# Kernel tuning notes

Hardware: AMD Instinct MI355X
Metric: run time of the kernel (lower is better)

Reference implementation:

```python
import jax, jax.numpy as jnp
import numpy as np

K = 20000   # know_num
I = 50000   # item_num
D = 128     # emb_dim
N = K + I   # nodes in exer+know graphs (exercises first)
E1 = 320000 # edges in directed knowledge graph
E2 = 640000 # edges in each exer<->know graph


def setup_inputs() -> dict:
    key = jax.random.key(0)
    ks = jax.random.split(key, 20)
    s = 1.0 / np.sqrt(D)
    s2 = 1.0 / np.sqrt(2 * D)
    return {
        'kn_emb': jax.random.normal(ks[0], (K, D), jnp.float32),
        'exer_emb': jax.random.normal(ks[1], (I, D), jnp.float32),
        # GAT params: W is fc.weight.T ([in,out]); a is attn_fc.weight flattened ([2D])
        'W_dir': jax.random.normal(ks[2], (D, D), jnp.float32) * s,
        'a_dir': jax.random.normal(ks[3], (2 * D,), jnp.float32) * s2,
        'W_ke': jax.random.normal(ks[4], (D, D), jnp.float32) * s,
        'a_ke': jax.random.normal(ks[5], (2 * D,), jnp.float32) * s2,
        'W_ek': jax.random.normal(ks[6], (D, D), jnp.float32) * s,
        'a_ek': jax.random.normal(ks[7], (2 * D,), jnp.float32) * s2,
        # relation attention MLP: Linear(D,D)+bias, Tanh, Linear(D,1,no bias)
        'rel_W1': jax.random.normal(ks[8], (D, D), jnp.float32) * s,
        'rel_b1': jax.random.normal(ks[9], (D,), jnp.float32) * s,
        'rel_w2': jax.random.normal(ks[10], (D,), jnp.float32) * s,
        # edge lists (src, dst)
        'directed_src': jax.random.randint(ks[11], (E1,), 0, K),
        'directed_dst': jax.random.randint(ks[12], (E1,), 0, K),
        'ke_src': jax.random.randint(ks[13], (E2,), 0, N),
        'ke_dst': jax.random.randint(ks[14], (E2,), 0, N),
        'ek_src': jax.random.randint(ks[15], (E2,), 0, N),
        'ek_dst': jax.random.randint(ks[16], (E2,), 0, N),
    }


def _gat(h, W, a, src, dst, n):
    # GraphLayer: z = fc(h); e = leaky_relu(attn_fc([z_src; z_dst]));
    # alpha = softmax_e over dst; h_out = sum alpha * z_src
    z = h @ W                                   # [n_in, D]
    # split attn vector: cat([z_src,z_dst]) @ a == z_src@a[:D] + z_dst@a[D:]
    s_src = z @ a[:D]                           # [n_in]
    s_dst = z @ a[D:]                           # [n_in]
    e = jax.nn.leaky_relu(s_src[src] + s_dst[dst], 0.01)  # [E]
    m = jax.ops.segment_max(e, dst, num_segments=n)
    ex = jnp.exp(e - m[dst])
    den = jax.ops.segment_sum(ex, dst, num_segments=n)
    alpha = ex / den[dst]                       # segment softmax over in-edges
    return jax.ops.segment_sum(alpha[:, None] * z[src], dst, num_segments=n)


def reference(kn_emb, exer_emb, W_dir, a_dir, W_ke, a_ke, W_ek, a_ek,
              rel_W1, rel_b1, rel_w2,
              directed_src, directed_dst, ke_src, ke_dst, ek_src, ek_dst):
    A = _gat(kn_emb, W_dir, a_dir, directed_src, directed_dst, K)      # [K,D]
    ek = jnp.concatenate([exer_emb, kn_emb], axis=0)                   # [N,D]
    B = _gat(ek, W_ke, a_ke, ke_src, ke_dst, N)[I:]                    # [K,D]
    Cfull = _gat(ek, W_ek, a_ek, ek_src, ek_dst, N)                    # [N,D]
    s1 = jnp.tanh(A @ rel_W1 + rel_b1) @ rel_w2                        # [K]
    s2 = jnp.tanh(B @ rel_W1 + rel_b1) @ rel_w2                        # [K]
    score = jax.nn.softmax(jnp.stack([s1, s2], axis=1), axis=1)        # [K,2]
    kn_out = score[:, 0:1] * A + score[:, 1:2] * B                     # [K,D]
    exer_out = Cfull[:I]                                               # [I,D]
    return (kn_out, exer_out)
```

## Files before the change

kernel.cpp:

```cpp
#include <hip/hip_runtime.h>
#include <math.h>

#define KN   20000
#define IN_  50000
#define DD   128
#define NN   70000
#define E1N  320000
#define E2N  640000

#define GB0  313
#define GB1  1094
#define GB2  1094
#define GTILES 2501

#define GROUPS 313
#define MGRID  (GROUPS*13)
#define CNT_CHUNKS 1563

typedef _Float16 f16x8 __attribute__((ext_vector_type(8)));
typedef float floatx4 __attribute__((ext_vector_type(4)));

__device__ __forceinline__ unsigned f2bf(float x) {
  unsigned u = __float_as_uint(x);
  return (u + 0x7FFFu + ((u >> 16) & 1u)) >> 16;
}
__device__ __forceinline__ unsigned packbf(float a, float b) {
  return f2bf(a) | (f2bf(b) << 16);
}
__device__ __forceinline__ float bf_lo(unsigned u) { return __uint_as_float(u << 16); }
__device__ __forceinline__ float bf_hi(unsigned u) { return __uint_as_float(u & 0xFFFF0000u); }

__global__ __launch_bounds__(256) void prep(
    const float* __restrict__ W0, const float* __restrict__ W1,
    const float* __restrict__ W2, const float* __restrict__ W3,
    short* __restrict__ wfr)
{
  int b = blockIdx.x;
  int wsel = b >> 3;
  const float* W = (wsel == 0) ? W0 : (wsel == 1) ? W1 : (wsel == 2) ? W2 : W3;
  int fi = (b & 7) * 256 + threadIdx.x;
  int l = fi & 63, chunk = (fi >> 6) & 3, t = fi >> 8;
  int col = t * 16 + (l & 15);
  int kbase = chunk * 32 + (l >> 4) * 8;
  f16x8 hv;
#pragma unroll
  for (int j = 0; j < 8; ++j) hv[j] = (_Float16)W[(kbase + j) * 128 + col];
  ((f16x8*)(wfr + wsel * 16384))[fi] = hv;
}

__global__ __launch_bounds__(256, 4) void gemm3_count(
    const float* __restrict__ kn, const float* __restrict__ ex,
    const short* __restrict__ wfr,
    const float* __restrict__ a_dir, const float* __restrict__ a_ke, const float* __restrict__ a_ek,
    unsigned* __restrict__ zb_dir, unsigned* __restrict__ zb_ke, unsigned* __restrict__ zb_ek,
    float* __restrict__ sds, float* __restrict__ sdd,
    float* __restrict__ sks, float* __restrict__ skd,
    float* __restrict__ ses, float* __restrict__ sed,
    const int* __restrict__ ddst, const int* __restrict__ kedst, const int* __restrict__ ekdst,
    int* __restrict__ cnt_dir, int* __restrict__ cnt_ke, int* __restrict__ cnt_ek,
    unsigned short* __restrict__ rank_dir, unsigned short* __restrict__ rank_ke,
    unsigned short* __restrict__ rank_ek)
{
  __shared__ short sW[16384];
  const int g = blockIdx.x / 13;
  const int r = blockIdx.x % 13;
  const int tid = threadIdx.x;

  if (r >= 8) {
    int cidx = g * 5 + (r - 8);
    if (cidx >= CNT_CHUNKS) return;
    int t = cidx * 256 + tid;
    if (t < 80000) {
      int e0 = t * 4;
      int4 d4 = *(const int4*)(ddst + e0);
      ushort4 rk;
      rk.x = (unsigned short)atomicAdd(&cnt_dir[d4.x], 1);
      rk.y = (unsigned short)atomicAdd(&cnt_dir[d4.y], 1);
      rk.z = (unsigned short)atomicAdd(&cnt_dir[d4.z], 1);
      rk.w = (unsigned short)atomicAdd(&cnt_dir[d4.w], 1);
      *(ushort4*)(rank_dir + e0) = rk;
    } else if (t < 240000) {
      int e0 = (t - 80000) * 4;
      int4 d4 = *(const int4*)(kedst + e0);
      ushort4 rk = make_ushort4(0, 0, 0, 0);
      if (d4.x >= IN_) rk.x = (unsigned short)atomicAdd(&cnt_ke[d4.x - IN_], 1);
      if (d4.y >= IN_) rk.y = (unsigned short)atomicAdd(&cnt_ke[d4.y - IN_], 1);
      if (d4.z >= IN_) rk.z = (unsigned short)atomicAdd(&cnt_ke[d4.z - IN_], 1);
      if (d4.w >= IN_) rk.w = (unsigned short)atomicAdd(&cnt_ke[d4.w - IN_], 1);
      *(ushort4*)(rank_ke + e0) = rk;
    } else if (t < 400000) {
      int e0 = (t - 240000) * 4;
      int4 d4 = *(const int4*)(ekdst + e0);
      ushort4 rk = make_ushort4(0, 0, 0, 0);
      if (d4.x < IN_) rk.x = (unsigned short)atomicAdd(&cnt_ek[d4.x], 1);
      if (d4.y < IN_) rk.y = (unsigned short)atomicAdd(&cnt_ek[d4.y], 1);
      if (d4.z < IN_) rk.z = (unsigned short)atomicAdd(&cnt_ek[d4.z], 1);
      if (d4.w < IN_) rk.w = (unsigned short)atomicAdd(&cnt_ek[d4.w], 1);
      *(ushort4*)(rank_ek + e0) = rk;
    }
    return;
  }

  const int bid = g * 8 + r;
  if (bid >= GTILES) return;

  const float *h1, *h2, *avec;
  unsigned* zb;
  float *ssrc, *sdst;
  const short* wf;
  int split, rows, tile;
  if (bid < GB0) {
    tile = bid; rows = KN; split = KN; h1 = kn; h2 = kn;
    wf = wfr; avec = a_dir; zb = zb_dir; ssrc = sds; sdst = sdd;
  } else if (bid < GB0 + GB1) {
    tile = bid - GB0; rows = NN; split = IN_; h1 = ex; h2 = kn;
    wf = wfr + 16384; avec = a_ke; zb = zb_ke; ssrc = sks; sdst = skd;
  } else {
    tile = bid - GB0 - GB1; rows = NN; split = IN_; h1 = ex; h2 = kn;
    wf = wfr + 32768; avec = a_ek; zb = zb_ek; ssrc = ses; sdst = sed;
  }

  {
    const int4* gs = (const int4*)wf;
    int4* ls = (int4*)sW;
#pragma unroll
    for (int it = 0; it < 8; ++it) ls[it * 256 + tid] = gs[it * 256 + tid];
  }
  __syncthreads();

  const int lane = tid & 63;
  const int wv = tid >> 6;
  const int q = lane >> 4;
  const int m = lane & 15;
  const int rr = tile * 64 + wv * 16 + m;
  const int rc = (rr < rows) ? rr : (rows - 1);
  const float* hp = (rc < split) ? (h1 + (size_t)rc * 128)
                                 : (h2 + (size_t)(rc - split) * 128);

  floatx4 acc[8];
#pragma unroll
  for (int t = 0; t < 8; ++t) { acc[t][0]=0.f; acc[t][1]=0.f; acc[t][2]=0.f; acc[t][3]=0.f; }

#pragma unroll
  for (int chunk = 0; chunk < 4; ++chunk) {
    float4 v0 = *(const float4*)(hp + chunk * 32 + q * 8);
    float4 v1 = *(const float4*)(hp + chunk * 32 + q * 8 + 4);
    float vs[8] = {v0.x, v0.y, v0.z, v0.w, v1.x, v1.y, v1.z, v1.w};
    f16x8 ahi, alo;
#pragma unroll
    for (int j = 0; j < 8; ++j) {
      _Float16 h = (_Float16)vs[j];
      ahi[j] = h;
      alo[j] = (_Float16)(vs[j] - (float)h);
    }
#pragma unroll
    for (int t = 0; t < 8; ++t) {
      f16x8 bh = ((const f16x8*)sW)[(t * 4 + chunk) * 64 + lane];
      acc[t] = __builtin_amdgcn_mfma_f32_16x16x32_f16(bh, ahi, acc[t], 0, 0, 0);
      acc[t] = __builtin_amdgcn_mfma_f32_16x16x32_f16(bh, alo, acc[t], 0, 0, 0);
    }
  }

  if (rr < rows) {
    unsigned* zrow = zb + (size_t)rr * 64;
#pragma unroll
    for (int t = 0; t < 8; ++t) {
      uint2 pk;
      pk.x = packbf(acc[t][0], acc[t][1]);
      pk.y = packbf(acc[t][2], acc[t][3]);
      *(uint2*)(zrow + t * 8 + q * 2) = pk;
    }
  }
  float d1 = 0.f, d2 = 0.f;
#pragma unroll
  for (int t = 0; t < 8; ++t) {
    float4 wa = *(const float4*)(avec + t * 16 + q * 4);
    float4 wb = *(const float4*)(avec + 128 + t * 16 + q * 4);
    d1 += acc[t][0] * wa.x + acc[t][1] * wa.y + acc[t][2] * wa.z + acc[t][3] * wa.w;
    d2 += acc[t][0] * wb.x + acc[t][1] * wb.y + acc[t][2] * wb.z + acc[t][3] * wb.w;
  }
  d1 += __shfl_xor(d1, 16, 64); d1 += __shfl_xor(d1, 32, 64);
  d2 += __shfl_xor(d2, 16, 64); d2 += __shfl_xor(d2, 32, 64);
  if (q == 0 && rr < rows) { ssrc[rr] = d1; sdst[rr] = d2; }
}

__global__ __launch_bounds__(256) void alloc_off(
    const int* __restrict__ cnt_dir, int2* __restrict__ sc_dir,
    const int* __restrict__ cnt_ke,  int2* __restrict__ sc_ke,
    const int* __restrict__ cnt_ek,  int2* __restrict__ sc_ek,
    int* __restrict__ totals)
{
  int b = blockIdx.x;
  const int* cnt; int2* sc; int* tot; int n, i0;
  if (b < 79)       { cnt = cnt_dir; sc = sc_dir; tot = totals + 0; n = KN;  i0 = b * 256; }
  else if (b < 158) { cnt = cnt_ke;  sc = sc_ke;  tot = totals + 1; n = KN;  i0 = (b - 79) * 256; }
  else              { cnt = cnt_ek;  sc = sc_ek;  tot = totals + 2; n = IN_; i0 = (b - 158) * 256; }
  int i = i0 + threadIdx.x;
  int lane = threadIdx.x & 63;
  int v = (i < n) ? cnt[i] : 0;
  int x = v;
#pragma unroll
  for (int o = 1; o < 64; o <<= 1) {
    int t = __shfl_up(x, o, 64);
    if (lane >= o) x += t;
  }
  int base = 0;
  if (lane == 63) base = atomicAdd(tot, x);
  base = __shfl(base, 63, 64);
  if (i < n) sc[i] = make_int2(base + x - v, v);
}

__global__ __launch_bounds__(256) void fill_edges(
    const int* __restrict__ dsrc, const int* __restrict__ ddst,
    const int* __restrict__ kesrc, const int* __restrict__ kedst,
    const int* __restrict__ eksrc, const int* __restrict__ ekdst,
    const unsigned short* __restrict__ rank_dir, const unsigned short* __restrict__ rank_ke,
    const unsigned short* __restrict__ rank_ek,
    const float* __restrict__ sds, const float* __restrict__ sdd,
    const float* __restrict__ sks, const float* __restrict__ skd,
    const float* __restrict__ ses, const float* __restrict__ sed,
    const int2* __restrict__ sc_dir, int2* __restrict__ ep_dir,
    const int2* __restrict__ sc_ke,  int2* __restrict__ ep_ke,
    const int2* __restrict__ sc_ek,  int2* __restrict__ ep_ek)
{
  int t = blockIdx.x * 256 + threadIdx.x;
  if (t < 80000) {
    int e0 = t * 4;
    int4 s4 = *(const int4*)(dsrc + e0);
    int4 d4 = *(const int4*)(ddst + e0);
    ushort4 rk = *(const ushort4*)(rank_dir + e0);
    ep_dir[sc_dir[d4.x].x + rk.x] = make_int2(s4.x, __float_as_int(sds[s4.x] + sdd[d4.x]));
    ep_dir[sc_dir[d4.y].x + rk.y] = make_int2(s4.y, __float_as_int(sds[s4.y] + sdd[d4.y]));
    ep_dir[sc_dir[d4.z].x + rk.z] = make_int2(s4.z, __float_as_int(sds[s4.z] + sdd[d4.z]));
    ep_dir[sc_dir[d4.w].x + rk.w] = make_int2(s4.w, __float_as_int(sds[s4.w] + sdd[d4.w]));
  } else if (t < 240000) {
    int e0 = (t - 80000) * 4;
    int4 s4 = *(const int4*)(kesrc + e0);
    int4 d4 = *(const int4*)(kedst + e0);
    ushort4 rk = *(const ushort4*)(rank_ke + e0);
    if (d4.x >= IN_) ep_ke[sc_ke[d4.x - IN_].x + rk.x] = make_int2(s4.x, __float_as_int(sks[s4.x] + skd[d4.x]));
    if (d4.y >= IN_) ep_ke[sc_ke[d4.y - IN_].x + rk.y] = make_int2(s4.y, __float_as_int(sks[s4.y] + skd[d4.y]));
    if (d4.z >= IN_) ep_ke[sc_ke[d4.z - IN_].x + rk.z] = make_int2(s4.z, __float_as_int(sks[s4.z] + skd[d4.z]));
    if (d4.w >= IN_) ep_ke[sc_ke[d4.w - IN_].x + rk.w] = make_int2(s4.w, __float_as_int(sks[s4.w] + skd[d4.w]));
  } else if (t < 400000) {
    int e0 = (t - 240000) * 4;
    int4 s4 = *(const int4*)(eksrc + e0);
    int4 d4 = *(const int4*)(ekdst + e0);
    ushort4 rk = *(const ushort4*)(rank_ek + e0);
    if (d4.x < IN_) ep_ek[sc_ek[d4.x].x + rk.x] = make_int2(s4.x, __float_as_int(ses[s4.x] + sed[d4.x]));
    if (d4.y < IN_) ep_ek[sc_ek[d4.y].x + rk.y] = make_int2(s4.y, __float_as_int(ses[s4.y] + sed[d4.y]));
    if (d4.z < IN_) ep_ek[sc_ek[d4.z].x + rk.z] = make_int2(s4.z, __float_as_int(ses[s4.z] + sed[d4.z]));
    if (d4.w < IN_) ep_ek[sc_ek[d4.w].x + rk.w] = make_int2(s4.w, __float_as_int(ses[s4.w] + sed[d4.w]));
  }
}

__global__ __launch_bounds__(256) void gat_gather(
    const int2* __restrict__ sc_dir, const int2* __restrict__ ep_dir,
    const unsigned* __restrict__ zb_dir, float* __restrict__ A,
    const int2* __restrict__ sc_ke, const int2* __restrict__ ep_ke,
    const unsigned* __restrict__ zb_ke, float* __restrict__ Bm,
    const int2* __restrict__ sc_ek, const int2* __restrict__ ep_ek,
    const unsigned* __restrict__ zb_ek, float* __restrict__ Cout)
{
  int gw = (blockIdx.x * 256 + threadIdx.x) >> 6;
  int lane = threadIdx.x & 63;
  int h = lane >> 5;
  int ln31 = lane & 31;
  int gh = (lane >> 4) & 1;
  int gl = lane & 15;

  const int2 *scp, *ep;
  const unsigned* zb;
  float* out;
  int s0;
  if (gw < 10000)      { s0 = 2 * gw;             scp = sc_dir; ep = ep_dir; zb = zb_dir; out = A; }
  else if (gw < 20000) { s0 = 2 * (gw - 10000);   scp = sc_ke;  ep = ep_ke;  zb = zb_ke;  out = Bm; }
  else                 { s0 = 2 * (gw - 20000);   scp = sc_ek;  ep = ep_ek;  zb = zb_ek;  out = Cout; }

  int4 scc = *(const int4*)((const int*)scp + 2 * s0);
  int b   = h ? scc.z : scc.x;
  int cnt = h ? scc.w : scc.y;
  int lim = (cnt < 32) ? cnt : 32;

  int   src_l = 0;
  float w_l   = 0.f;
  if (ln31 < lim) {
    int2 pe = ep[b + ln31];
    src_l = pe.x;
    float x = __int_as_float(pe.y);
    x = (x > 0.f) ? x : 0.01f * x;
    w_l = __expf(x);
  }

  float den = w_l;
  den += __shfl_xor(den, 1, 64);
  den += __shfl_xor(den, 2, 64);
  den += __shfl_xor(den, 4, 64);
  den += __shfl_xor(den, 8, 64);
  den += __shfl_xor(den, 16, 64);

  float av[8];
#pragma unroll
  for (int k = 0; k < 8; ++k) av[k] = 0.f;

  for (int j0 = 0; j0 < lim; j0 += 8) {
    int base = h * 32 + j0 + gh * 4;
    int   s1 = __shfl(src_l, base + 0, 64); float w1 = __shfl(w_l, base + 0, 64);
    int   s2 = __shfl(src_l, base + 1, 64); float w2 = __shfl(w_l, base + 1, 64);
    int   s3 = __shfl(src_l, base + 2, 64); float w3 = __shfl(w_l, base + 2, 64);
    int   s4 = __shfl(src_l, base + 3, 64); float w4 = __shfl(w_l, base + 3, 64);
    uint4 za = *(const uint4*)(zb + (size_t)s1 * 64 + gl * 4);
    uint4 zc = *(const uint4*)(zb + (size_t)s2 * 64 + gl * 4);
    uint4 ze = *(const uint4*)(zb + (size_t)s3 * 64 + gl * 4);
    uint4 zg = *(const uint4*)(zb + (size_t)s4 * 64 + gl * 4);
    av[0] += w1 * bf_lo(za.x); av[1] += w1 * bf_hi(za.x);
    av[2] += w1 * bf_lo(za.y); av[3] += w1 * bf_hi(za.y);
    av[4] += w1 * bf_lo(za.z); av[5] += w1 * bf_hi(za.z);
    av[6] += w1 * bf_lo(za.w); av[7] += w1 * bf_hi(za.w);
    av[0] += w2 * bf_lo(zc.x); av[1] += w2 * bf_hi(zc.x);
    av[2] += w2 * bf_lo(zc.y); av[3] += w2 * bf_hi(zc.y);
    av[4] += w2 * bf_lo(zc.z); av[5] += w2 * bf_hi(zc.z);
    av[6] += w2 * bf_lo(zc.w); av[7] += w2 * bf_hi(zc.w);
    av[0] += w3 * bf_lo(ze.x); av[1] += w3 * bf_hi(ze.x);
    av[2] += w3 * bf_lo(ze.y); av[3] += w3 * bf_hi(ze.y);
    av[4] += w3 * bf_lo(ze.z); av[5] += w3 * bf_hi(ze.z);
    av[6] += w3 * bf_lo(ze.w); av[7] += w3 * bf_hi(ze.w);
    av[0] += w4 * bf_lo(zg.x); av[1] += w4 * bf_hi(zg.x);
    av[2] += w4 * bf_lo(zg.y); av[3] += w4 * bf_hi(zg.y);
    av[4] += w4 * bf_lo(zg.z); av[5] += w4 * bf_hi(zg.z);
    av[6] += w4 * bf_lo(zg.w); av[7] += w4 * bf_hi(zg.w);
  }

  if (cnt > 32) {
    float dtail = 0.f;
    int e = b + cnt;
    for (int i = b + 32 + gh; i < e; i += 2) {
      int2 p1 = ep[i];
      float x1 = __int_as_float(p1.y);
      x1 = (x1 > 0.f) ? x1 : 0.01f * x1;
      float w1 = __expf(x1);
      uint4 za = *(const uint4*)(zb + (size_t)p1.x * 64 + gl * 4);
      dtail += w1;
      av[0] += w1 * bf_lo(za.x); av[1] += w1 * bf_hi(za.x);
      av[2] += w1 * bf_lo(za.y); av[3] += w1 * bf_hi(za.y);
      av[4] += w1 * bf_lo(za.z); av[5] += w1 * bf_hi(za.z);
      av[6] += w1 * bf_lo(za.w); av[7] += w1 * bf_hi(za.w);
    }
    den += dtail + __shfl_xor(dtail, 16, 64);
  }

#pragma unroll
  for (int k = 0; k < 8; ++k) av[k] += __shfl_xor(av[k], 16, 64);

  if (cnt > 0) {
    float inv = 1.f / den;
#pragma unroll
    for (int k = 0; k < 8; ++k) av[k] *= inv;
  }

  if (gh == 0) {
    int seg = s0 + h;
    float* op = out + (size_t)seg * 128 + gl * 8;
    *(float4*)op       = make_float4(av[0], av[1], av[2], av[3]);
    *(float4*)(op + 4) = make_float4(av[4], av[5], av[6], av[7]);
  }
}

__global__ __launch_bounds__(256, 2) void relgemm_combine(
    const float* __restrict__ Am, const float* __restrict__ Bm,
    const short* __restrict__ wfr_rel,
    const float* __restrict__ rb1, const float* __restrict__ rw2,
    float* __restrict__ out)
{
  __shared__ short sW[16384];
  const int tid = threadIdx.x;
  {
    const int4* gs = (const int4*)wfr_rel;
    int4* ls = (int4*)sW;
#pragma unroll
    for (int it = 0; it < 8; ++it) ls[it * 256 + tid] = gs[it * 256 + tid];
  }
  __syncthreads();

  const int lane = tid & 63;
  const int wv = tid >> 6;
  const int q = lane >> 4;
  const int m = lane & 15;
  const int r = blockIdx.x * 64 + wv * 16 + m;
  const int rc = (r < KN) ? r : (KN - 1);
  const float* hA = Am + (size_t)rc * 128;
  const float* hB = Bm + (size_t)rc * 128;

  floatx4 accA[8], accB[8];
#pragma unroll
  for (int t = 0; t < 8; ++t) {
    accA[t][0]=0.f; accA[t][1]=0.f; accA[t][2]=0.f; accA[t][3]=0.f;
    accB[t][0]=0.f; accB[t][1]=0.f; accB[t][2]=0.f; accB[t][3]=0.f;
  }

#pragma unroll
  for (int chunk = 0; chunk < 4; ++chunk) {
    float4 a0 = *(const float4*)(hA + chunk * 32 + q * 8);
    float4 a1 = *(const float4*)(hA + chunk * 32 + q * 8 + 4);
    float4 b0 = *(const float4*)(hB + chunk * 32 + q * 8);
    float4 b1 = *(const float4*)(hB + chunk * 32 + q * 8 + 4);
    float as[8] = {a0.x, a0.y, a0.z, a0.w, a1.x, a1.y, a1.z, a1.w};
    float bs[8] = {b0.x, b0.y, b0.z, b0.w, b1.x, b1.y, b1.z, b1.w};
    f16x8 ahiA, aloA, ahiB, aloB;
#pragma unroll
    for (int j = 0; j < 8; ++j) {
      _Float16 ha = (_Float16)as[j];
      ahiA[j] = ha; aloA[j] = (_Float16)(as[j] - (float)ha);
      _Float16 hb = (_Float16)bs[j];
      ahiB[j] = hb; aloB[j] = (_Float16)(bs[j] - (float)hb);
    }
#pragma unroll
    for (int t = 0; t < 8; ++t) {
      f16x8 bh = ((const f16x8*)sW)[(t * 4 + chunk) * 64 + lane];
      accA[t] = __builtin_amdgcn_mfma_f32_16x16x32_f16(bh, ahiA, accA[t], 0, 0, 0);
      accA[t] = __builtin_amdgcn_mfma_f32_16x16x32_f16(bh, aloA, accA[t], 0, 0, 0);
      accB[t] = __builtin_amdgcn_mfma_f32_16x16x32_f16(bh, ahiB, accB[t], 0, 0, 0);
      accB[t] = __builtin_amdgcn_mfma_f32_16x16x32_f16(bh, aloB, accB[t], 0, 0, 0);
    }
  }

  float p1 = 0.f, p2 = 0.f;
#pragma unroll
  for (int t = 0; t < 8; ++t) {
    float4 bb = *(const float4*)(rb1 + t * 16 + q * 4);
    float4 ww = *(const float4*)(rw2 + t * 16 + q * 4);
    p1 += tanhf(accA[t][0] + bb.x) * ww.x + tanhf(accA[t][1] + bb.y) * ww.y +
          tanhf(accA[t][2] + bb.z) * ww.z + tanhf(accA[t][3] + bb.w) * ww.w;
    p2 += tanhf(accB[t][0] + bb.x) * ww.x + tanhf(accB[t][1] + bb.y) * ww.y +
          tanhf(accB[t][2] + bb.z) * ww.z + tanhf(accB[t][3] + bb.w) * ww.w;
  }
  p1 += __shfl_xor(p1, 16, 64); p1 += __shfl_xor(p1, 32, 64);
  p2 += __shfl_xor(p2, 16, 64); p2 += __shfl_xor(p2, 32, 64);

  float mx = fmaxf(p1, p2);
  float e1 = __expf(p1 - mx), e2 = __expf(p2 - mx);
  float al = e1 / (e1 + e2), be = e2 / (e1 + e2);

  if (r < KN) {
#pragma unroll
    for (int t = 0; t < 8; ++t) {
      int col = t * 16 + q * 4;
      float4 avv = *(const float4*)(Am + (size_t)r * 128 + col);
      float4 bvv = *(const float4*)(Bm + (size_t)r * 128 + col);
      *(float4*)(out + (size_t)r * 128 + col) =
          make_float4(al * avv.x + be * bvv.x, al * avv.y + be * bvv.y,
                      al * avv.z + be * bvv.z, al * avv.w + be * bvv.w);
    }
  }
}

extern "C" void kernel_launch(void* const* d_in, const int* in_sizes, int n_in,
                              void* d_out, int out_size, void* d_ws, size_t ws_size,
                              hipStream_t stream) {
  const float* kn    = (const float*)d_in[0];
  const float* ex    = (const float*)d_in[1];
  const float* W_dir = (const float*)d_in[2];
  const float* a_dir = (const float*)d_in[3];
  const float* W_ke  = (const float*)d_in[4];
  const float* a_ke  = (const float*)d_in[5];
  const float* W_ek  = (const float*)d_in[6];
  const float* a_ek  = (const float*)d_in[7];
  const float* rW1   = (const float*)d_in[8];
  const float* rb1   = (const float*)d_in[9];
  const float* rw2   = (const float*)d_in[10];
  const int* dsrc    = (const int*)d_in[11];
  const int* ddst    = (const int*)d_in[12];
  const int* kesrc   = (const int*)d_in[13];
  const int* kedst   = (const int*)d_in[14];
  const int* eksrc   = (const int*)d_in[15];
  const int* ekdst   = (const int*)d_in[16];
  float* out = (float*)d_out;

  char* p = (char*)d_ws;
  auto alloc = [&](size_t bytes) {
    char* r = p;
    p += (bytes + 255) & ~(size_t)255;
    return r;
  };
  unsigned* zb_dir = (unsigned*)alloc((size_t)KN * 64 * 4);
  unsigned* zb_ke  = (unsigned*)alloc((size_t)NN * 64 * 4);
  unsigned* zb_ek  = (unsigned*)alloc((size_t)NN * 64 * 4);
  float* Am    = (float*)alloc((size_t)KN * 128 * 4);
  float* Bmat  = (float*)alloc((size_t)KN * 128 * 4);
  short* wfr   = (short*)alloc((size_t)4 * 16384 * 2);
  float* sds = (float*)alloc(KN * 4);
  float* sdd = (float*)alloc(KN * 4);
  float* sks = (float*)alloc(NN * 4);
  float* skd = (float*)alloc(NN * 4);
  float* ses = (float*)alloc(NN * 4);
  float* sed = (float*)alloc(NN * 4);
  int* cntblk  = (int*)alloc((size_t)(2 * KN + IN_ + 64) * 4);
  int* cnt_dir = cntblk;
  int* cnt_ke  = cntblk + KN;
  int* cnt_ek  = cntblk + 2 * KN;
  int* totals  = cntblk + 2 * KN + IN_;
  int2* sc_dir = (int2*)alloc((size_t)KN * 8);
  int2* sc_ke  = (int2*)alloc((size_t)KN * 8);
  int2* sc_ek  = (int2*)alloc((size_t)IN_ * 8);
  unsigned short* rank_dir = (unsigned short*)alloc((size_t)E1N * 2);
  unsigned short* rank_ke  = (unsigned short*)alloc((size_t)E2N * 2);
  unsigned short* rank_ek  = (unsigned short*)alloc((size_t)E2N * 2);
  int2* ep_dir = (int2*)alloc((size_t)E1N * 8);
  int2* ep_ke  = (int2*)alloc((size_t)E2N * 8);
  int2* ep_ek  = (int2*)alloc((size_t)E2N * 8);

  hipMemsetAsync(cntblk, 0, (size_t)(2 * KN + IN_ + 64) * 4, stream);

  prep<<<32, 256, 0, stream>>>(W_dir, W_ke, W_ek, rW1, wfr);

  gemm3_count<<<MGRID, 256, 0, stream>>>(
      kn, ex, wfr, a_dir, a_ke, a_ek,
      zb_dir, zb_ke, zb_ek,
      sds, sdd, sks, skd, ses, sed,
      ddst, kedst, ekdst, cnt_dir, cnt_ke, cnt_ek,
      rank_dir, rank_ke, rank_ek);

  alloc_off<<<354, 256, 0, stream>>>(cnt_dir, sc_dir, cnt_ke, sc_ke, cnt_ek, sc_ek, totals);

  fill_edges<<<1563, 256, 0, stream>>>(
      dsrc, ddst, kesrc, kedst, eksrc, ekdst,
      rank_dir, rank_ke, rank_ek,
      sds, sdd, sks, skd, ses, sed,
      sc_dir, ep_dir, sc_ke, ep_ke, sc_ek, ep_ek);

  gat_gather<<<11250, 256, 0, stream>>>(
      sc_dir, ep_dir, zb_dir, Am,
      sc_ke,  ep_ke,  zb_ke,  Bmat,
      sc_ek,  ep_ek,  zb_ek,  out + (size_t)KN * 128);

  relgemm_combine<<<313, 256, 0, stream>>>(Am, Bmat, wfr + 3 * 16384, rb1, rw2, out);
}
```

Before: 262.3 us.

## Privatize per-destination edge counters into 8 copies and use fast tanh

The degree-count atomics are spread across 8 private counter arrays chosen by block index, with the copy id packed into the high bits of the stored rank. The offset kernel then prefix-sums the 8 copies per destination and writes a start offset for each copy, which the edge-fill kernel uses to place edges. This is meant to cut atomic contention on hot destination counters, at the cost of a larger memset, more counter memory and extra offset reads. tanhf in the relation scorer is also swapped for a clamped exp-based approximation.

```diff
diff --git a/kernel.cpp b/kernel.cpp
--- a/kernel.cpp
+++ b/kernel.cpp
@@ -17,6 +17,11 @@
 #define MGRID  (GROUPS*13)
 #define CNT_CHUNKS 1563
 
+#define CP_DIR 0
+#define CP_KE  160000
+#define CP_EK  320000
+#define CNT2_INTS 720000
+
 typedef _Float16 f16x8 __attribute__((ext_vector_type(8)));
 typedef float floatx4 __attribute__((ext_vector_type(4)));
 
@@ -29,6 +34,12 @@
 }
 __device__ __forceinline__ float bf_lo(unsigned u) { return __uint_as_float(u << 16); }
 __device__ __forceinline__ float bf_hi(unsigned u) { return __uint_as_float(u & 0xFFFF0000u); }
+
+__device__ __forceinline__ float ftanh(float x) {
+  x = fminf(15.f, fmaxf(-15.f, x));
+  float t = __expf(2.f * x);
+  return (t - 1.f) / (t + 1.f);
+}
 
 __global__ __launch_bounds__(256) void prep(
     const float* __restrict__ W0, const float* __restrict__ W1,
@@ -57,7 +68,7 @@
     float* __restrict__ sks, float* __restrict__ skd,
     float* __restrict__ ses, float* __restrict__ sed,
     const int* __restrict__ ddst, const int* __restrict__ kedst, const int* __restrict__ ekdst,
-    int* __restrict__ cnt_dir, int* __restrict__ cnt_ke, int* __restrict__ cnt_ek,
+    int* __restrict__ cnt2,
     unsigned short* __restrict__ rank_dir, unsigned short* __restrict__ rank_ke,
     unsigned short* __restrict__ rank_ek)
 {
@@ -69,33 +80,38 @@
   if (r >= 8) {
     int cidx = g * 5 + (r - 8);
     if (cidx >= CNT_CHUNKS) return;
+    const int r7 = blockIdx.x & 7;
+    const unsigned rtag = (unsigned)r7 << 12;
     int t = cidx * 256 + tid;
     if (t < 80000) {
       int e0 = t * 4;
       int4 d4 = *(const int4*)(ddst + e0);
+      int* cp = cnt2 + CP_DIR + r7 * 20000;
       ushort4 rk;
-      rk.x = (unsigned short)atomicAdd(&cnt_dir[d4.x], 1);
-      rk.y = (unsigned short)atomicAdd(&cnt_dir[d4.y], 1);
-      rk.z = (unsigned short)atomicAdd(&cnt_dir[d4.z], 1);
-      rk.w = (unsigned short)atomicAdd(&cnt_dir[d4.w], 1);
+      rk.x = (unsigned short)(atomicAdd(&cp[d4.x], 1) | rtag);
+      rk.y = (unsigned short)(atomicAdd(&cp[d4.y], 1) | rtag);
+      rk.z = (unsigned short)(atomicAdd(&cp[d4.z], 1) | rtag);
+      rk.w = (unsigned short)(atomicAdd(&cp[d4.w], 1) | rtag);
       *(ushort4*)(rank_dir + e0) = rk;
     } else if (t < 240000) {
       int e0 = (t - 80000) * 4;
       int4 d4 = *(const int4*)(kedst + e0);
+      int* cp = cnt2 + CP_KE + r7 * 20000;
       ushort4 rk = make_ushort4(0, 0, 0, 0);
-      if (d4.x >= IN_) rk.x = (unsigned short)atomicAdd(&cnt_ke[d4.x - IN_], 1);
-      if (d4.y >= IN_) rk.y = (unsigned short)atomicAdd(&cnt_ke[d4.y - IN_], 1);
-      if (d4.z >= IN_) rk.z = (unsigned short)atomicAdd(&cnt_ke[d4.z - IN_], 1);
-      if (d4.w >= IN_) rk.w = (unsigned short)atomicAdd(&cnt_ke[d4.w - IN_], 1);
+      if (d4.x >= IN_) rk.x = (unsigned short)(atomicAdd(&cp[d4.x - IN_], 1) | rtag);
+      if (d4.y >= IN_) rk.y = (unsigned short)(atomicAdd(&cp[d4.y - IN_], 1) | rtag);
+      if (d4.z >= IN_) rk.z = (unsigned short)(atomicAdd(&cp[d4.z - IN_], 1) | rtag);
+      if (d4.w >= IN_) rk.w = (unsigned short)(atomicAdd(&cp[d4.w - IN_], 1) | rtag);
       *(ushort4*)(rank_ke + e0) = rk;
     } else if (t < 400000) {
       int e0 = (t - 240000) * 4;
       int4 d4 = *(const int4*)(ekdst + e0);
+      int* cp = cnt2 + CP_EK + r7 * 50000;
       ushort4 rk = make_ushort4(0, 0, 0, 0);
-      if (d4.x < IN_) rk.x = (unsigned short)atomicAdd(&cnt_ek[d4.x], 1);
-      if (d4.y < IN_) rk.y = (unsigned short)atomicAdd(&cnt_ek[d4.y], 1);
-      if (d4.z < IN_) rk.z = (unsigned short)atomicAdd(&cnt_ek[d4.z], 1);
-      if (d4.w < IN_) rk.w = (unsigned short)atomicAdd(&cnt_ek[d4.w], 1);
+      if (d4.x < IN_) rk.x = (unsigned short)(atomicAdd(&cp[d4.x], 1) | rtag);
+      if (d4.y < IN_) rk.y = (unsigned short)(atomicAdd(&cp[d4.y], 1) | rtag);
+      if (d4.z < IN_) rk.z = (unsigned short)(atomicAdd(&cp[d4.z], 1) | rtag);
+      if (d4.w < IN_) rk.w = (unsigned short)(atomicAdd(&cp[d4.w], 1) | rtag);
       *(ushort4*)(rank_ek + e0) = rk;
     }
     return;
@@ -185,19 +201,27 @@
 }
 
 __global__ __launch_bounds__(256) void alloc_off(
-    const int* __restrict__ cnt_dir, int2* __restrict__ sc_dir,
-    const int* __restrict__ cnt_ke,  int2* __restrict__ sc_ke,
-    const int* __restrict__ cnt_ek,  int2* __restrict__ sc_ek,
+    const int* __restrict__ cnt2, int* __restrict__ st2,
+    int2* __restrict__ sc_dir, int2* __restrict__ sc_ke, int2* __restrict__ sc_ek,
     int* __restrict__ totals)
 {
   int b = blockIdx.x;
-  const int* cnt; int2* sc; int* tot; int n, i0;
-  if (b < 79)       { cnt = cnt_dir; sc = sc_dir; tot = totals + 0; n = KN;  i0 = b * 256; }
-  else if (b < 158) { cnt = cnt_ke;  sc = sc_ke;  tot = totals + 1; n = KN;  i0 = (b - 79) * 256; }
-  else              { cnt = cnt_ek;  sc = sc_ek;  tot = totals + 2; n = IN_; i0 = (b - 158) * 256; }
+  const int* cp; int* sp; int2* sc; int* tot; int n, i0;
+  if (b < 79)       { cp = cnt2 + CP_DIR; sp = st2 + CP_DIR; sc = sc_dir; tot = totals + 0; n = 20000; i0 = b * 256; }
+  else if (b < 158) { cp = cnt2 + CP_KE;  sp = st2 + CP_KE;  sc = sc_ke;  tot = totals + 1; n = 20000; i0 = (b - 79) * 256; }
+  else              { cp = cnt2 + CP_EK;  sp = st2 + CP_EK;  sc = sc_ek;  tot = totals + 2; n = 50000; i0 = (b - 158) * 256; }
   int i = i0 + threadIdx.x;
   int lane = threadIdx.x & 63;
-  int v = (i < n) ? cnt[i] : 0;
+
+  int pre[8];
+  int v = 0;
+#pragma unroll
+  for (int r = 0; r < 8; ++r) {
+    int c = (i < n) ? cp[r * n + i] : 0;
+    pre[r] = v;
+    v += c;
+  }
+
   int x = v;
 #pragma unroll
   for (int o = 1; o < 64; o <<= 1) {
@@ -207,7 +231,12 @@
   int base = 0;
   if (lane == 63) base = atomicAdd(tot, x);
   base = __shfl(base, 63, 64);
-  if (i < n) sc[i] = make_int2(base + x - v, v);
+  int start = base + x - v;
+  if (i < n) {
+    sc[i] = make_int2(start, v);
+#pragma unroll
+    for (int r = 0; r < 8; ++r) sp[r * n + i] = start + pre[r];
+  }
 }
 
 __global__ __launch_bounds__(256) void fill_edges(
@@ -219,9 +248,8 @@
     const float* __restrict__ sds, const float* __restrict__ sdd,
     const float* __restrict__ sks, const float* __restrict__ skd,
     const float* __restrict__ ses, const float* __restrict__ sed,
-    const int2* __restrict__ sc_dir, int2* __restrict__ ep_dir,
-    const int2* __restrict__ sc_ke,  int2* __restrict__ ep_ke,
-    const int2* __restrict__ sc_ek,  int2* __restrict__ ep_ek)
+    const int* __restrict__ st2,
+    int2* __restrict__ ep_dir, int2* __restrict__ ep_ke, int2* __restrict__ ep_ek)
 {
   int t = blockIdx.x * 256 + threadIdx.x;
   if (t < 80000) {
@@ -229,28 +257,31 @@
     int4 s4 = *(const int4*)(dsrc + e0);
     int4 d4 = *(const int4*)(ddst + e0);
     ushort4 rk = *(const ushort4*)(rank_dir + e0);
-    ep_dir[sc_dir[d4.x].x + rk.x] = make_int2(s4.x, __float_as_int(sds[s4.x] + sdd[d4.x]));
-    ep_dir[sc_dir[d4.y].x + rk.y] = make_int2(s4.y, __float_as_int(sds[s4.y] + sdd[d4.y]));
-    ep_dir[sc_dir[d4.z].x + rk.z] = make_int2(s4.z, __float_as_int(sds[s4.z] + sdd[d4.z]));
-    ep_dir[sc_dir[d4.w].x + rk.w] = make_int2(s4.w, __float_as_int(sds[s4.w] + sdd[d4.w]));
+    const int* sp = st2 + CP_DIR;
+    ep_dir[sp[(rk.x >> 12) * 20000 + d4.x] + (rk.x & 0xFFF)] = make_int2(s4.x, __float_as_int(sds[s4.x] + sdd[d4.x]));
+    ep_dir[sp[(rk.y >> 12) * 20000 + d4.y] + (rk.y & 0xFFF)] = make_int2(s4.y, __float_as_int(sds[s4.y] + sdd[d4.y]));
+    ep_dir[sp[(rk.z >> 12) * 20000 + d4.z] + (rk.z & 0xFFF)] = make_int2(s4.z, __float_as_int(sds[s4.z] + sdd[d4.z]));
+    ep_dir[sp[(rk.w >> 12) * 20000 + d4.w] + (rk.w & 0xFFF)] = make_int2(s4.w, __float_as_int(sds[s4.w] + sdd[d4.w]));
   } else if (t < 240000) {
     int e0 = (t - 80000) * 4;
     int4 s4 = *(const int4*)(kesrc + e0);
     int4 d4 = *(const int4*)(kedst + e0);
     ushort4 rk = *(const ushort4*)(rank_ke + e0);
-    if (d4.x >= IN_) ep_ke[sc_ke[d4.x - IN_].x + rk.x] = make_int2(s4.x, __float_as_int(sks[s4.x] + skd[d4.x]));
-    if (d4.y >= IN_) ep_ke[sc_ke[d4.y - IN_].x + rk.y] = make_int2(s4.y, __float_as_int(sks[s4.y] + skd[d4.y]));
-    if (d4.z >= IN_) ep_ke[sc_ke[d4.z - IN_].x + rk.z] = make_int2(s4.z, __float_as_int(sks[s4.z] + skd[d4.z]));
-    if (d4.w >= IN_) ep_ke[sc_ke[d4.w - IN_].x + rk.w] = make_int2(s4.w, __float_as_int(sks[s4.w] + skd[d4.w]));
+    const int* sp = st2 + CP_KE;
+    if (d4.x >= IN_) ep_ke[sp[(rk.x >> 12) * 20000 + d4.x - IN_] + (rk.x & 0xFFF)] = make_int2(s4.x, __float_as_int(sks[s4.x] + skd[d4.x]));
+    if (d4.y >= IN_) ep_ke[sp[(rk.y >> 12) * 20000 + d4.y - IN_] + (rk.y & 0xFFF)] = make_int2(s4.y, __float_as_int(sks[s4.y] + skd[d4.y]));
+    if (d4.z >= IN_) ep_ke[sp[(rk.z >> 12) * 20000 + d4.z - IN_] + (rk.z & 0xFFF)] = make_int2(s4.z, __float_as_int(sks[s4.z] + skd[d4.z]));
+    if (d4.w >= IN_) ep_ke[sp[(rk.w >> 12) * 20000 + d4.w - IN_] + (rk.w & 0xFFF)] = make_int2(s4.w, __float_as_int(sks[s4.w] + skd[d4.w]));
   } else if (t < 400000) {
     int e0 = (t - 240000) * 4;
     int4 s4 = *(const int4*)(eksrc + e0);
     int4 d4 = *(const int4*)(ekdst + e0);
     ushort4 rk = *(const ushort4*)(rank_ek + e0);
-    if (d4.x < IN_) ep_ek[sc_ek[d4.x].x + rk.x] = make_int2(s4.x, __float_as_int(ses[s4.x] + sed[d4.x]));
-    if (d4.y < IN_) ep_ek[sc_ek[d4.y].x + rk.y] = make_int2(s4.y, __float_as_int(ses[s4.y] + sed[d4.y]));
-    if (d4.z < IN_) ep_ek[sc_ek[d4.z].x + rk.z] = make_int2(s4.z, __float_as_int(ses[s4.z] + sed[d4.z]));
-    if (d4.w < IN_) ep_ek[sc_ek[d4.w].x + rk.w] = make_int2(s4.w, __float_as_int(ses[s4.w] + sed[d4.w]));
+    const int* sp = st2 + CP_EK;
+    if (d4.x < IN_) ep_ek[sp[(rk.x >> 12) * 50000 + d4.x] + (rk.x & 0xFFF)] = make_int2(s4.x, __float_as_int(ses[s4.x] + sed[d4.x]));
+    if (d4.y < IN_) ep_ek[sp[(rk.y >> 12) * 50000 + d4.y] + (rk.y & 0xFFF)] = make_int2(s4.y, __float_as_int(ses[s4.y] + sed[d4.y]));
+    if (d4.z < IN_) ep_ek[sp[(rk.z >> 12) * 50000 + d4.z] + (rk.z & 0xFFF)] = make_int2(s4.z, __float_as_int(ses[s4.z] + sed[d4.z]));
+    if (d4.w < IN_) ep_ek[sp[(rk.w >> 12) * 50000 + d4.w] + (rk.w & 0xFFF)] = make_int2(s4.w, __float_as_int(ses[s4.w] + sed[d4.w]));
   }
 }
 
@@ -429,10 +460,10 @@
   for (int t = 0; t < 8; ++t) {
     float4 bb = *(const float4*)(rb1 + t * 16 + q * 4);
     float4 ww = *(const float4*)(rw2 + t * 16 + q * 4);
-    p1 += tanhf(accA[t][0] + bb.x) * ww.x + tanhf(accA[t][1] + bb.y) * ww.y +
-          tanhf(accA[t][2] + bb.z) * ww.z + tanhf(accA[t][3] + bb.w) * ww.w;
-    p2 += tanhf(accB[t][0] + bb.x) * ww.x + tanhf(accB[t][1] + bb.y) * ww.y +
-          tanhf(accB[t][2] + bb.z) * ww.z + tanhf(accB[t][3] + bb.w) * ww.w;
+    p1 += ftanh(accA[t][0] + bb.x) * ww.x + ftanh(accA[t][1] + bb.y) * ww.y +
+          ftanh(accA[t][2] + bb.z) * ww.z + ftanh(accA[t][3] + bb.w) * ww.w;
+    p2 += ftanh(accB[t][0] + bb.x) * ww.x + ftanh(accB[t][1] + bb.y) * ww.y +
+          ftanh(accB[t][2] + bb.z) * ww.z + ftanh(accB[t][3] + bb.w) * ww.w;
   }
   p1 += __shfl_xor(p1, 16, 64); p1 += __shfl_xor(p1, 32, 64);
   p2 += __shfl_xor(p2, 16, 64); p2 += __shfl_xor(p2, 32, 64);
@@ -494,11 +525,9 @@
   float* skd = (float*)alloc(NN * 4);
   float* ses = (float*)alloc(NN * 4);
   float* sed = (float*)alloc(NN * 4);
-  int* cntblk  = (int*)alloc((size_t)(2 * KN + IN_ + 64) * 4);
-  int* cnt_dir = cntblk;
-  int* cnt_ke  = cntblk + KN;
-  int* cnt_ek  = cntblk + 2 * KN;
-  int* totals  = cntblk + 2 * KN + IN_;
+  int* cnt2 = (int*)alloc((size_t)(CNT2_INTS + 64) * 4);
+  int* totals = cnt2 + CNT2_INTS;
+  int* st2  = (int*)alloc((size_t)CNT2_INTS * 4);
   int2* sc_dir = (int2*)alloc((size_t)KN * 8);
   int2* sc_ke  = (int2*)alloc((size_t)KN * 8);
   int2* sc_ek  = (int2*)alloc((size_t)IN_ * 8);
@@ -509,7 +538,7 @@
   int2* ep_ke  = (int2*)alloc((size_t)E2N * 8);
   int2* ep_ek  = (int2*)alloc((size_t)E2N * 8);
 
-  hipMemsetAsync(cntblk, 0, (size_t)(2 * KN + IN_ + 64) * 4, stream);
+  hipMemsetAsync(cnt2, 0, (size_t)(CNT2_INTS + 64) * 4, stream);
 
   prep<<<32, 256, 0, stream>>>(W_dir, W_ke, W_ek, rW1, wfr);
 
@@ -517,16 +546,16 @@
       kn, ex, wfr, a_dir, a_ke, a_ek,
       zb_dir, zb_ke, zb_ek,
       sds, sdd, sks, skd, ses, sed,
-      ddst, kedst, ekdst, cnt_dir, cnt_ke, cnt_ek,
+      ddst, kedst, ekdst, cnt2,
       rank_dir, rank_ke, rank_ek);
 
-  alloc_off<<<354, 256, 0, stream>>>(cnt_dir, sc_dir, cnt_ke, sc_ke, cnt_ek, sc_ek, totals);
+  alloc_off<<<354, 256, 0, stream>>>(cnt2, st2, sc_dir, sc_ke, sc_ek, totals);
 
   fill_edges<<<1563, 256, 0, stream>>>(
       dsrc, ddst, kesrc, kedst, eksrc, ekdst,
       rank_dir, rank_ke, rank_ek,
       sds, sdd, sks, skd, ses, sed,
-      sc_dir, ep_dir, sc_ke, ep_ke, sc_ek, ep_ek);
+      st2, ep_dir, ep_ke, ep_ek);
 
   gat_gather<<<11250, 256, 0, stream>>>(
       sc_dir, ep_dir, zb_dir, Am,
```

Measured after the change: 260.1 us. Within noise of the previous version (-0.8%).
